# Kernel optimization log

Hardware: AMD Instinct MI355X
Metric: run time of the kernel (lower is better)

Reference implementation:

```python
import jax, jax.numpy as jnp
import numpy as np
import math

SIX = 6
LUT_SCALE = 50
DEPTH = 2048
BATCH = 2048


def _build_tables(depth):
    # p_q_2_lut_table[j, i] = 1 if bit j of i is 1; [j+SIX, i] = 1 if bit j is 0.
    table = np.zeros((2 * SIX, 2 ** SIX), dtype=np.float32)
    lut = np.zeros((depth, 2 ** SIX), dtype=np.float32)
    for i in range(2 ** SIX):
        bins = ('{0:0%db}' % SIX).format(i)
        for j in range(SIX):
            if bins[j] == '0':
                table[j + SIX, i] = 1.0
            else:
                table[j, i] = 1.0
        a = bins.count('0') / SIX
        a = 0.01 if a == 0 else (0.99 if a == 1 else a)
        lut[:, i] = math.log(a / (1 - a)) / LUT_SCALE
    return jnp.asarray(table), jnp.asarray(lut)


def setup_inputs() -> dict:
    key = jax.random.key(0)
    inputs = jax.random.uniform(key, (BATCH, DEPTH, SIX), dtype=jnp.float32)
    p_q_2_lut_table, lut = _build_tables(DEPTH)
    return {"inputs": inputs, "lut": lut, "p_q_2_lut_table": p_q_2_lut_table}


def reference(inputs, lut, p_q_2_lut_table):
    eps = 1e-07
    # torch: repeat along new dim then overwrite channel 0 with 1-x; flattening
    # (2, SIX) -> 12 puts the (1-x) block first, then the x block.
    p_q = jnp.concatenate([1.0 - inputs, inputs], axis=-1)        # (B, D, 12)
    p_q = jax.nn.relu(p_q) + eps
    lut_p = jnp.exp(jnp.log(p_q) @ p_q_2_lut_table)               # (B, D, 64)
    gate = jax.nn.sigmoid(lut * LUT_SCALE)                        # (D, 64)
    return jnp.sum(lut_p * gate, axis=-1)                         # (B, D)
```

## Files before the change

kernel.cpp:

```cpp
#include <hip/hip_runtime.h>

#define DDIM 2048
#define BDIM 2048
#define EPS 1e-7f
#define DPB 256
#define B_CHUNK 16
#define B_SUB 4
#define NSTAGE (B_CHUNK / B_SUB)

__global__ __launch_bounds__(256)
void lut_layer_kernel(const float* __restrict__ inputs,
                      const float* __restrict__ lut,
                      float* __restrict__ out) {
    __shared__ float sbuf[B_SUB * DPB * 6];

    const int t    = threadIdx.x;
    const int lane = t & 63;
    const int wrow = t >> 6;
    const int d0   = blockIdx.x * DPB;
    const int b0   = blockIdx.y * B_CHUNK;

    float g[64];
    {
        const float4* lr = reinterpret_cast<const float4*>(lut + (size_t)(d0 + t) * 64);
#pragma unroll
        for (int k = 0; k < 16; ++k) {
            float4 v = lr[k];
            g[4*k+0] = 1.0f / (1.0f + __expf(-50.0f * v.x));
            g[4*k+1] = 1.0f / (1.0f + __expf(-50.0f * v.y));
            g[4*k+2] = 1.0f / (1.0f + __expf(-50.0f * v.z));
            g[4*k+3] = 1.0f / (1.0f + __expf(-50.0f * v.w));
        }
    }

    const float*  gbase = inputs + ((size_t)b0 * DDIM + d0) * 6;
    const size_t  rstr  = (size_t)DDIM * 6;

    float4 pf[6];
    auto LOAD_STAGE = [&](int s) {
#pragma unroll
        for (int r = 0; r < 6; ++r)
            pf[r] = *reinterpret_cast<const float4*>(
                gbase + (size_t)(s * B_SUB + wrow) * rstr + ((r * 64 + lane) << 2));
    };
    auto WRITE_STAGE = [&]() {
#pragma unroll
        for (int r = 0; r < 6; ++r)
            *reinterpret_cast<float4*>(
                &sbuf[wrow * (DPB * 6) + ((r * 64 + lane) << 2)]) = pf[r];
    };

    LOAD_STAGE(0);
    WRITE_STAGE();
    __syncthreads();

    float* op = out + (size_t)b0 * DDIM + d0 + t;

    for (int s = 0; s < NSTAGE; ++s) {
        if (s + 1 < NSTAGE) LOAD_STAGE(s + 1);

#pragma unroll
        for (int bl = 0; bl < B_SUB; ++bl) {
            const float* e = &sbuf[bl * (DPB * 6) + t * 6];
            float x0 = e[0], x1 = e[1], x2 = e[2], x3 = e[3], x4 = e[4], x5 = e[5];

            float lo0 = fmaxf(x0, 0.f) + EPS, hi0 = fmaxf(1.f - x0, 0.f) + EPS;
            float lo1 = fmaxf(x1, 0.f) + EPS, hi1 = fmaxf(1.f - x1, 0.f) + EPS;
            float lo2 = fmaxf(x2, 0.f) + EPS, hi2 = fmaxf(1.f - x2, 0.f) + EPS;
            float lo3 = fmaxf(x3, 0.f) + EPS, hi3 = fmaxf(1.f - x3, 0.f) + EPS;
            float lo4 = fmaxf(x4, 0.f) + EPS, hi4 = fmaxf(1.f - x4, 0.f) + EPS;
            float lo5 = fmaxf(x5, 0.f) + EPS, hi5 = fmaxf(1.f - x5, 0.f) + EPS;

            float m01[4] = {lo0 * lo1, lo0 * hi1, hi0 * lo1, hi0 * hi1};
            float m23[4] = {lo2 * lo3, lo2 * hi3, hi2 * lo3, hi2 * hi3};
            float m45[4] = {lo4 * lo5, lo4 * hi5, hi4 * lo5, hi4 * hi5};

            float acc = 0.f;
#pragma unroll
            for (int p = 0; p < 4; ++p) {
                float accp = 0.f;
#pragma unroll
                for (int q = 0; q < 4; ++q) {
                    const int base = p * 16 + q * 4;
                    float inner = m45[0] * g[base + 0];
                    inner = fmaf(m45[1], g[base + 1], inner);
                    inner = fmaf(m45[2], g[base + 2], inner);
                    inner = fmaf(m45[3], g[base + 3], inner);
                    accp = fmaf(m23[q], inner, accp);
                }
                acc = fmaf(m01[p], accp, acc);
            }
            __builtin_nontemporal_store(acc, op + (size_t)(s * B_SUB + bl) * DDIM);
        }
        __syncthreads();
        if (s + 1 < NSTAGE) {
            WRITE_STAGE();
            __syncthreads();
        }
    }
}

extern "C" void kernel_launch(void* const* d_in, const int* in_sizes, int n_in,
                              void* d_out, int out_size, void* d_ws, size_t ws_size,
                              hipStream_t stream) {
    const float* inputs = (const float*)d_in[0];
    const float* lut    = (const float*)d_in[1];
    float* out = (float*)d_out;

    dim3 grid(DDIM / DPB, BDIM / B_CHUNK);
    dim3 block(256);
    lut_layer_kernel<<<grid, block, 0, stream>>>(inputs, lut, out);
}
```

Baseline: 185.4 us.

## Make staging wave-private to drop barriers and precompute sigmoid gate once

Each wavefront now owns a private LDS slice covering its own 64 depth columns, so the block-wide __syncthreads around the staging buffer are removed. The sigmoid of the LUT is precomputed by a separate kernel into the workspace when space allows, so each block no longer repeats 64 exps per thread. The batch chunk and sub-chunk are halved, which doubles the grid and spreads the per-block gate load over fewer rows, and launch bounds request four blocks per SIMD. Costs are an extra kernel launch and more redundant gate reads per output row.

```diff
diff --git a/kernel.cpp b/kernel.cpp
--- a/kernel.cpp
+++ b/kernel.cpp
@@ -4,64 +4,86 @@
 #define BDIM 2048
 #define EPS 1e-7f
 #define DPB 256
-#define B_CHUNK 16
-#define B_SUB 4
+#define B_CHUNK 8
+#define B_SUB 2
 #define NSTAGE (B_CHUNK / B_SUB)
+#define GATE_BYTES (DDIM * 64 * sizeof(float))
 
 __global__ __launch_bounds__(256)
+void gate_kernel(const float* __restrict__ lut, float* __restrict__ gate) {
+    const int i = blockIdx.x * 256 + threadIdx.x;
+    float4 v = reinterpret_cast<const float4*>(lut)[i];
+    float4 r;
+    r.x = 1.0f / (1.0f + __expf(-50.0f * v.x));
+    r.y = 1.0f / (1.0f + __expf(-50.0f * v.y));
+    r.z = 1.0f / (1.0f + __expf(-50.0f * v.z));
+    r.w = 1.0f / (1.0f + __expf(-50.0f * v.w));
+    reinterpret_cast<float4*>(gate)[i] = r;
+}
+
+template <bool INLINE_GATE>
+__global__ __launch_bounds__(256, 4)
 void lut_layer_kernel(const float* __restrict__ inputs,
-                      const float* __restrict__ lut,
+                      const float* __restrict__ gsrc,
                       float* __restrict__ out) {
-    __shared__ float sbuf[B_SUB * DPB * 6];
-
+    __shared__ float sbuf[4][B_SUB][64 * 6];
     const int t    = threadIdx.x;
     const int lane = t & 63;
-    const int wrow = t >> 6;
+    const int w    = t >> 6;
     const int d0   = blockIdx.x * DPB;
     const int b0   = blockIdx.y * B_CHUNK;
+    const int dme  = d0 + w * 64 + lane;
 
     float g[64];
     {
-        const float4* lr = reinterpret_cast<const float4*>(lut + (size_t)(d0 + t) * 64);
+        const float4* gr = reinterpret_cast<const float4*>(gsrc + (size_t)dme * 64);
 #pragma unroll
         for (int k = 0; k < 16; ++k) {
-            float4 v = lr[k];
-            g[4*k+0] = 1.0f / (1.0f + __expf(-50.0f * v.x));
-            g[4*k+1] = 1.0f / (1.0f + __expf(-50.0f * v.y));
-            g[4*k+2] = 1.0f / (1.0f + __expf(-50.0f * v.z));
-            g[4*k+3] = 1.0f / (1.0f + __expf(-50.0f * v.w));
+            float4 v = gr[k];
+            if (INLINE_GATE) {
+                g[4*k+0] = 1.0f / (1.0f + __expf(-50.0f * v.x));
+                g[4*k+1] = 1.0f / (1.0f + __expf(-50.0f * v.y));
+                g[4*k+2] = 1.0f / (1.0f + __expf(-50.0f * v.z));
+                g[4*k+3] = 1.0f / (1.0f + __expf(-50.0f * v.w));
+            } else {
+                g[4*k+0] = v.x; g[4*k+1] = v.y; g[4*k+2] = v.z; g[4*k+3] = v.w;
+            }
         }
     }
 
-    const float*  gbase = inputs + ((size_t)b0 * DDIM + d0) * 6;
-    const size_t  rstr  = (size_t)DDIM * 6;
+    const float* gbase = inputs + ((size_t)b0 * DDIM + d0 + w * 64) * 6;
+    const size_t rstr  = (size_t)DDIM * 6;
+    float* const lds   = &sbuf[w][0][0];
 
-    float4 pf[6];
+    float4 pfA[B_SUB];
+    float2 pfB[B_SUB];
     auto LOAD_STAGE = [&](int s) {
 #pragma unroll
-        for (int r = 0; r < 6; ++r)
-            pf[r] = *reinterpret_cast<const float4*>(
-                gbase + (size_t)(s * B_SUB + wrow) * rstr + ((r * 64 + lane) << 2));
+        for (int r = 0; r < B_SUB; ++r) {
+            const float* src = gbase + (size_t)(s * B_SUB + r) * rstr;
+            pfA[r] = *reinterpret_cast<const float4*>(src + lane * 4);
+            pfB[r] = *reinterpret_cast<const float2*>(src + 256 + lane * 2);
+        }
     };
     auto WRITE_STAGE = [&]() {
 #pragma unroll
-        for (int r = 0; r < 6; ++r)
-            *reinterpret_cast<float4*>(
-                &sbuf[wrow * (DPB * 6) + ((r * 64 + lane) << 2)]) = pf[r];
+        for (int r = 0; r < B_SUB; ++r) {
+            float* dst = lds + r * (64 * 6);
+            *reinterpret_cast<float4*>(dst + lane * 4)       = pfA[r];
+            *reinterpret_cast<float2*>(dst + 256 + lane * 2) = pfB[r];
+        }
     };
 
     LOAD_STAGE(0);
     WRITE_STAGE();
-    __syncthreads();
 
-    float* op = out + (size_t)b0 * DDIM + d0 + t;
-
+#pragma unroll
     for (int s = 0; s < NSTAGE; ++s) {
         if (s + 1 < NSTAGE) LOAD_STAGE(s + 1);
 
 #pragma unroll
-        for (int bl = 0; bl < B_SUB; ++bl) {
-            const float* e = &sbuf[bl * (DPB * 6) + t * 6];
+        for (int r = 0; r < B_SUB; ++r) {
+            const float* e = lds + r * (64 * 6) + lane * 6;
             float x0 = e[0], x1 = e[1], x2 = e[2], x3 = e[3], x4 = e[4], x5 = e[5];
 
             float lo0 = fmaxf(x0, 0.f) + EPS, hi0 = fmaxf(1.f - x0, 0.f) + EPS;
@@ -90,13 +112,10 @@
                 }
                 acc = fmaf(m01[p], accp, acc);
             }
-            __builtin_nontemporal_store(acc, op + (size_t)(s * B_SUB + bl) * DDIM);
+            __builtin_nontemporal_store(
+                acc, out + (size_t)(b0 + s * B_SUB + r) * DDIM + d0 + w * 64 + lane);
         }
-        __syncthreads();
-        if (s + 1 < NSTAGE) {
-            WRITE_STAGE();
-            __syncthreads();
-        }
+        if (s + 1 < NSTAGE) WRITE_STAGE();
     }
 }
 
@@ -106,8 +125,14 @@
     const float* inputs = (const float*)d_in[0];
     const float* lut    = (const float*)d_in[1];
     float* out = (float*)d_out;
-
     dim3 grid(DDIM / DPB, BDIM / B_CHUNK);
     dim3 block(256);
-    lut_layer_kernel<<<grid, block, 0, stream>>>(inputs, lut, out);
+
+    if (ws_size >= GATE_BYTES) {
+        float* gate = (float*)d_ws;
+        gate_kernel<<<dim3(DDIM * 64 / 4 / 256), block, 0, stream>>>(lut, gate);
+        lut_layer_kernel<false><<<grid, block, 0, stream>>>(inputs, gate, out);
+    } else {
+        lut_layer_kernel<true><<<grid, block, 0, stream>>>(inputs, lut, out);
+    }
 }
```

After: 186.6 us. No clear change (+0.6%).
